# Kernel tuning notes

Measured on AMD Instinct MI355X. Metric: run time of the kernel, lower is better.

The kernel has to match this reference:

```python
import jax, jax.numpy as jnp
import numpy as np

B, L, E, H, D = 4, 2048, 2048, 16, 128
HALF = D // 2
EPS = 1e-6


def setup_inputs() -> dict:
    key = jax.random.key(0)
    ks = jax.random.split(key, 8)
    s = 1.0 / np.sqrt(E)
    x = jax.random.normal(ks[0], (B, L, E), dtype=jnp.float32)
    # causal boolean mask, True = attend
    attention_mask = jnp.tril(jnp.ones((L, L), dtype=bool))[None, None, :, :]
    attention_mask = jnp.broadcast_to(attention_mask, (B, 1, L, L))
    pos = jnp.arange(L, dtype=jnp.float32)[:, None]
    inv_freq = 1.0 / (10000.0 ** (jnp.arange(HALF, dtype=jnp.float32) / HALF))
    ang = pos * inv_freq[None, :]  # [L, HALF]
    cos = jnp.broadcast_to(jnp.cos(ang)[None], (B, L, HALF)).astype(jnp.float32)
    sin = jnp.broadcast_to(jnp.sin(ang)[None], (B, L, HALF)).astype(jnp.float32)
    Wq = jax.random.normal(ks[1], (H * D, E), dtype=jnp.float32) * s
    Wk = jax.random.normal(ks[2], (H * D, E), dtype=jnp.float32) * s
    Wv = jax.random.normal(ks[3], (H * D, E), dtype=jnp.float32) * s
    Wo = jax.random.normal(ks[4], (E, H * D), dtype=jnp.float32) * s
    q_norm_w = jnp.ones((D,), dtype=jnp.float32)
    k_norm_w = jnp.ones((D,), dtype=jnp.float32)
    return {"x": x, "attention_mask": attention_mask, "cos": cos, "sin": sin,
            "Wq": Wq, "Wk": Wk, "Wv": Wv, "Wo": Wo,
            "q_norm_w": q_norm_w, "k_norm_w": k_norm_w}


def _rmsnorm(t, w):
    # t: [B,H,L,D]; matches torch: x / sqrt(mean(x^2) + eps) * w
    ms = jnp.mean(t * t, axis=-1, keepdims=True)
    return w * (t * jax.lax.rsqrt(ms + EPS))


def _rope(t, cos, sin):
    # t: [B,H,L,D]; cos/sin: [B,L,HALF] -> [B,1,L,HALF]
    c = cos[:, None, :, :]
    s = sin[:, None, :, :]
    t1, t2 = t[..., :HALF], t[..., HALF:]
    return jnp.concatenate([t1 * c - t2 * s, t1 * s + t2 * c], axis=-1)


def reference(x, attention_mask, cos, sin, Wq, Wk, Wv, Wo, q_norm_w, k_norm_w):
    b, l, _ = x.shape
    q = (x @ Wq.T).reshape(b, l, H, D).transpose(0, 2, 1, 3)  # [B,H,L,D]
    k = (x @ Wk.T).reshape(b, l, H, D).transpose(0, 2, 1, 3)
    v = (x @ Wv.T).reshape(b, l, H, D).transpose(0, 2, 1, 3)
    q = _rope(_rmsnorm(q, q_norm_w), cos, sin)
    k = _rope(_rmsnorm(k, k_norm_w), cos, sin)
    scale = 1.0 / jnp.sqrt(jnp.asarray(D, dtype=x.dtype))
    scores = jnp.einsum('bhld,bhmd->bhlm', q, k) * scale  # [B,H,L,L]
    scores = jnp.where(attention_mask, scores, -jnp.inf)
    attn = jax.nn.softmax(scores, axis=-1)
    out = jnp.einsum('bhlm,bhmd->bhld', attn, v)  # [B,H,L,D]
    out = out.transpose(0, 2, 1, 3).reshape(b, l, H * D)
    return out @ Wo.T
```

## Files before the change

kernel.cpp:

```cpp
#include <hip/hip_runtime.h>
#include <hip/hip_bf16.h>
#include <stdint.h>

#define B_SZ 4
#define L_SEQ 2048
#define EMB 2048
#define NH 16
#define HD 128
#define BLROWS (B_SZ * L_SEQ)
#define BK 32

typedef __bf16 bf16;
typedef __bf16 bf16x8 __attribute__((ext_vector_type(8)));
typedef __bf16 bf16x4 __attribute__((ext_vector_type(4)));
typedef float f32x4 __attribute__((ext_vector_type(4)));

#define MFMA16(A, Bv, C) __builtin_amdgcn_mfma_f32_16x16x32_bf16(A, Bv, C, 0, 0, 0)

__device__ __forceinline__ void gll16(bf16* l, const bf16* g) {
  __builtin_amdgcn_global_load_lds(
      (const __attribute__((address_space(1))) unsigned int*)g,
      (__attribute__((address_space(3))) unsigned int*)l, 16, 0, 0);
}

__global__ __launch_bounds__(256) void f2b_kernel(const float* __restrict__ in,
                                                  bf16* __restrict__ out, int n4) {
  int i = blockIdx.x * blockDim.x + threadIdx.x;
  int stride = gridDim.x * blockDim.x;
  for (; i < n4; i += stride) {
    float4 v = ((const float4*)in)[i];
    bf16x4 o = {(bf16)v.x, (bf16)v.y, (bf16)v.z, (bf16)v.w};
    ((bf16x4*)out)[i] = o;
  }
}

template <int EPI>
__global__ __launch_bounds__(512, 2) void gemm256(const bf16* __restrict__ A,
                                                  const bf16* __restrict__ Bm,
                                                  bf16* __restrict__ Cq,
                                                  bf16* __restrict__ Ck,
                                                  bf16* __restrict__ Cvt,
                                                  float* __restrict__ Cf,
                                                  int K) {
  __shared__ bf16 Abuf[3][256 * BK];
  __shared__ bf16 Bbuf[3][256 * BK];
  const int tid = threadIdx.x, lane = tid & 63, w = tid >> 6;
  const int wr = w >> 2, wc = w & 3;
  const int l15 = lane & 15;

  const int q8 = gridDim.x >> 3;
  const int wg = ((int)blockIdx.x & 7) * q8 + ((int)blockIdx.x >> 3);
  const int bm = (wg & 31) * 256;
  const int bn = (wg >> 5) * 256;
  const int NT = K / BK;

  const int idA0 = tid, idA1 = 512 + tid;
  const int ar0 = idA0 >> 2, ar1 = idA1 >> 2;
  const size_t aS0 = (size_t)(bm + ar0) * K + (((idA0 & 3) ^ ((ar0 >> 1) & 3)) * 8);
  const size_t aS1 = (size_t)(bm + ar1) * K + (((idA1 & 3) ^ ((ar1 >> 1) & 3)) * 8);
  const size_t bS0 = (size_t)(bn + ar0) * K + (((idA0 & 3) ^ ((ar0 >> 1) & 3)) * 8);
  const size_t bS1 = (size_t)(bn + ar1) * K + (((idA1 & 3) ^ ((ar1 >> 1) & 3)) * 8);
  const int ldsD0 = idA0 * 8, ldsD1 = idA1 * 8;

  const int eSw = ((lane >> 4) * 8) ^ (((l15 >> 1) & 3) << 3);
  int aoff[8], boff[4];
#pragma unroll
  for (int m = 0; m < 8; m++) aoff[m] = (wr * 128 + m * 16 + l15) * BK + eSw;
#pragma unroll
  for (int n = 0; n < 4; n++) boff[n] = (wc * 64 + n * 16 + l15) * BK + eSw;

  f32x4 acc[8][4] = {};

  gll16(&Abuf[0][ldsD0], A + aS0);
  gll16(&Bbuf[0][ldsD0], Bm + bS0);
  gll16(&Abuf[0][ldsD1], A + aS1);
  gll16(&Bbuf[0][ldsD1], Bm + bS1);
  gll16(&Abuf[1][ldsD0], A + aS0 + BK);
  gll16(&Bbuf[1][ldsD0], Bm + bS0 + BK);
  gll16(&Abuf[1][ldsD1], A + aS1 + BK);
  gll16(&Bbuf[1][ldsD1], Bm + bS1 + BK);
  asm volatile("s_waitcnt vmcnt(4)" ::: "memory");
  __builtin_amdgcn_s_barrier();
  asm volatile("" ::: "memory");

  int cur = 0, nxt = 2;
  for (int kt = 0; kt < NT; ++kt) {
    const bf16* __restrict__ Ab = Abuf[cur];
    const bf16* __restrict__ Bb = Bbuf[cur];
    const bool pre = (kt + 2 < NT);
    const size_t k2 = (size_t)(kt + 2) * BK;

    bf16x8 af[8], b0, b1;
#pragma unroll
    for (int m = 0; m < 8; m++) af[m] = *(const bf16x8*)&Ab[aoff[m]];
    b0 = *(const bf16x8*)&Bb[boff[0]];
    b1 = *(const bf16x8*)&Bb[boff[1]];
    if (pre) {
      gll16(&Abuf[nxt][ldsD0], A + aS0 + k2);
      gll16(&Bbuf[nxt][ldsD0], Bm + bS0 + k2);
    }
    asm volatile("s_waitcnt lgkmcnt(0)" ::: "memory");
    __builtin_amdgcn_sched_barrier(0);
    __builtin_amdgcn_s_setprio(1);
#pragma unroll
    for (int m = 0; m < 8; m++) acc[m][0] = MFMA16(af[m], b0, acc[m][0]);
#pragma unroll
    for (int m = 0; m < 8; m++) acc[m][1] = MFMA16(af[m], b1, acc[m][1]);
    __builtin_amdgcn_s_setprio(0);

    bf16x8 b2 = *(const bf16x8*)&Bb[boff[2]];
    bf16x8 b3 = *(const bf16x8*)&Bb[boff[3]];
    if (pre) {
      gll16(&Abuf[nxt][ldsD1], A + aS1 + k2);
      gll16(&Bbuf[nxt][ldsD1], Bm + bS1 + k2);
    }
    asm volatile("s_waitcnt lgkmcnt(0)" ::: "memory");
    __builtin_amdgcn_sched_barrier(0);
    __builtin_amdgcn_s_setprio(1);
#pragma unroll
    for (int m = 0; m < 8; m++) acc[m][2] = MFMA16(af[m], b2, acc[m][2]);
#pragma unroll
    for (int m = 0; m < 8; m++) acc[m][3] = MFMA16(af[m], b3, acc[m][3]);
    __builtin_amdgcn_s_setprio(0);

    if (kt < NT - 1) {
      if (pre)
        asm volatile("s_waitcnt vmcnt(4)" ::: "memory");
      else
        asm volatile("s_waitcnt vmcnt(0)" ::: "memory");
      __builtin_amdgcn_s_barrier();
      asm volatile("" ::: "memory");
    }
    cur = (cur == 2) ? 0 : cur + 1;
    nxt = (nxt == 2) ? 0 : nxt + 1;
  }

  const int grow0 = bm + wr * 128 + (lane >> 4) * 4;
  const int gcol0 = bn + wc * 64 + l15;
#pragma unroll
  for (int i = 0; i < 8; i++)
#pragma unroll
    for (int j = 0; j < 4; j++) {
      int grow = grow0 + i * 16;
      int gcol = gcol0 + j * 16;
      if (EPI == 1) {
#pragma unroll
        for (int r = 0; r < 4; r++)
          Cf[(size_t)(grow + r) * 2048 + gcol] = acc[i][j][r];
      } else {
        int mat = gcol >> 11, mcol = gcol & 2047;
        if (mat == 2) {
          int b = grow >> 11;
          bf16x4 pk = {(bf16)acc[i][j][0], (bf16)acc[i][j][1],
                       (bf16)acc[i][j][2], (bf16)acc[i][j][3]};
          *(bf16x4*)&Cvt[((size_t)(b * 2048 + mcol)) * 2048 + (grow & 2047)] = pk;
        } else {
          bf16* Cp = (mat == 0) ? Cq : Ck;
#pragma unroll
          for (int r = 0; r < 4; r++)
            Cp[(size_t)(grow + r) * 2048 + mcol] = (bf16)acc[i][j][r];
        }
      }
    }
}

__global__ __launch_bounds__(256) void normrope_kernel(bf16* __restrict__ T,
                                                       const float* __restrict__ w,
                                                       const float* __restrict__ cs,
                                                       const float* __restrict__ sn) {
  int row = blockIdx.x * 4 + (threadIdx.x >> 6);
  int lane = threadIdx.x & 63;
  int bl = row >> 4;
  int h = row & 15;
  bf16* p = T + (size_t)bl * EMB + h * HD;
  float v1 = (float)p[lane];
  float v2 = (float)p[lane + 64];
  float ss = v1 * v1 + v2 * v2;
#pragma unroll
  for (int m = 32; m; m >>= 1) ss += __shfl_xor(ss, m, 64);
  float r = rsqrtf(ss * (1.0f / 128.0f) + 1e-6f);
  float n1 = v1 * r * w[lane];
  float n2 = v2 * r * w[lane + 64];
  float c = cs[(size_t)bl * 64 + lane];
  float s = sn[(size_t)bl * 64 + lane];
  p[lane]      = (bf16)(n1 * c - n2 * s);
  p[lane + 64] = (bf16)(n1 * s + n2 * c);
}

__device__ __forceinline__ void stage_kv(bf16* Ksb, bf16* Vsb,
                                         const bf16* gK, const bf16* gV,
                                         int kt, int w, int lane) {
#pragma unroll
  for (int i = 0; i < 4; i++) {
    int ck = i * 256 + w * 64 + lane;
    int kr = ck >> 4, kc = ck & 15;
    gll16(&Ksb[ck * 8], gK + (size_t)(kt * 64 + kr) * EMB + ((kc ^ (kr & 7)) * 8));
    int dr = ck >> 3, vc = ck & 7;
    gll16(&Vsb[ck * 8], gV + (size_t)dr * L_SEQ + kt * 64 + ((vc ^ (dr & 7)) * 8));
  }
}

__global__ __launch_bounds__(256) void fattn_kernel(const bf16* __restrict__ Q,
                                                    const bf16* __restrict__ K,
                                                    const bf16* __restrict__ Vt,
                                                    bf16* __restrict__ AO) {
  __shared__ bf16 Ks[2][64 * 128];
  __shared__ bf16 Vs[2][64 * 128];
  __shared__ bf16 Ps[4 * 32 * 64];
  const int tid = threadIdx.x, lane = tid & 63, w = tid >> 6;
  const int l15 = lane & 15;

  int id = blockIdx.x + blockIdx.y * 16;
  int bh = id & 63;
  int qti = 15 - (id >> 6);
  const int b = bh >> 4, h = bh & 15;
  const size_t base = (size_t)b * L_SEQ * EMB + h * HD;
  const bf16* gK = K + base;
  const bf16* gV = Vt + (size_t)(b * NH + h) * HD * L_SEQ;
  const int qrow0 = qti * 128 + w * 32;

  const float a_ = 0.08838834764831845f * 1.4426950408889634f;
  const float b_ = 12.0f * 1.4426950408889634f;

  bf16x8 qf[2][4];
#pragma unroll
  for (int mi = 0; mi < 2; mi++) {
    const bf16* qp = Q + base + (size_t)(qrow0 + mi * 16 + l15) * EMB + ((lane >> 4) * 8);
#pragma unroll
    for (int c = 0; c < 4; c++) qf[mi][c] = *(const bf16x8*)(qp + c * 32);
  }
  const bf16 one1 = (bf16)1.0f;
  const bf16x8 ones = {one1, one1, one1, one1, one1, one1, one1, one1};

  f32x4 O[2][8] = {};
  f32x4 lsum[2] = {};
  const int prow = (lane >> 4) * 4;
  bf16* myP = Ps + w * 2048;

  const int nkt = 2 * qti + 2;
  stage_kv(Ks[0], Vs[0], gK, gV, 0, w, lane);
  asm volatile("s_waitcnt vmcnt(0)" ::: "memory");
  __builtin_amdgcn_s_barrier();
  asm volatile("" ::: "memory");

  for (int kt = 0; kt < nkt; kt++) {
    const int cur = kt & 1;
    if (kt + 1 < nkt) stage_kv(Ks[cur ^ 1], Vs[cur ^ 1], gK, gV, kt + 1, w, lane);

    const bool active = (kt * 64 <= qrow0 + 31);
    if (active) {
      f32x4 S[2][4] = {};
      __builtin_amdgcn_s_setprio(1);
#pragma unroll
      for (int s = 0; s < 4; s++) {
        int row = s * 16 + l15;
#pragma unroll
        for (int c = 0; c < 4; c++) {
          int swc = (c * 4 + (lane >> 4)) ^ (row & 7);
          bf16x8 kf = *(const bf16x8*)&Ks[cur][row * 128 + swc * 8];
          S[0][s] = MFMA16(qf[0][c], kf, S[0][s]);
          S[1][s] = MFMA16(qf[1][c], kf, S[1][s]);
        }
      }
      __builtin_amdgcn_s_setprio(0);

#pragma unroll
      for (int mi = 0; mi < 2; mi++)
#pragma unroll
        for (int s = 0; s < 4; s++) {
          int kg = kt * 64 + s * 16 + l15;
#pragma unroll
          for (int r = 0; r < 4; r++) {
            int qg = qrow0 + mi * 16 + prow + r;
            float e = exp2f(S[mi][s][r] * a_ - b_);
            if (kg > qg) e = 0.f;
            int row = mi * 16 + prow + r;
            myP[(row * 64 + s * 16 + l15) ^ ((row & 7) << 3)] = (bf16)e;
          }
        }
      bf16x8 pf[2][2];
#pragma unroll
      for (int mi = 0; mi < 2; mi++)
#pragma unroll
        for (int kk = 0; kk < 2; kk++) {
          int row = mi * 16 + l15;
          int swc = (kk * 4 + (lane >> 4)) ^ (row & 7);
          pf[mi][kk] = *(const bf16x8*)&myP[row * 64 + swc * 8];
        }
      __builtin_amdgcn_s_setprio(1);
#pragma unroll
      for (int mi = 0; mi < 2; mi++) {
        lsum[mi] = MFMA16(pf[mi][0], ones, lsum[mi]);
        lsum[mi] = MFMA16(pf[mi][1], ones, lsum[mi]);
      }
#pragma unroll
      for (int ni = 0; ni < 8; ni++) {
#pragma unroll
        for (int kk = 0; kk < 2; kk++) {
          int drow = ni * 16 + l15;
          int swc = (kk * 4 + (lane >> 4)) ^ (drow & 7);
          bf16x8 vf = *(const bf16x8*)&Vs[cur][drow * 64 + swc * 8];
          O[0][ni] = MFMA16(pf[0][kk], vf, O[0][ni]);
          O[1][ni] = MFMA16(pf[1][kk], vf, O[1][ni]);
        }
      }
      __builtin_amdgcn_s_setprio(0);
    }

    asm volatile("s_waitcnt vmcnt(0)" ::: "memory");
    __builtin_amdgcn_s_barrier();
    asm volatile("" ::: "memory");
  }

#pragma unroll
  for (int mi = 0; mi < 2; mi++)
#pragma unroll
    for (int ni = 0; ni < 8; ni++) {
#pragma unroll
      for (int r = 0; r < 4; r++) {
        float o = O[mi][ni][r] / lsum[mi][r];
        int grow = qrow0 + mi * 16 + prow + r;
        AO[(size_t)(b * L_SEQ + grow) * EMB + h * HD + ni * 16 + l15] = (bf16)o;
      }
    }
}

extern "C" void kernel_launch(void* const* d_in, const int* in_sizes, int n_in,
                              void* d_out, int out_size, void* d_ws, size_t ws_size,
                              hipStream_t stream) {
  const float* x = (const float*)d_in[0];
  const float* cosp = (const float*)d_in[2];
  const float* sinp = (const float*)d_in[3];
  const float* Wq = (const float*)d_in[4];
  const float* Wk = (const float*)d_in[5];
  const float* Wv = (const float*)d_in[6];
  const float* Wo = (const float*)d_in[7];
  const float* qw = (const float*)d_in[8];
  const float* kw = (const float*)d_in[9];

  const size_t ACT = (size_t)BLROWS * EMB * sizeof(bf16);
  const size_t WGT = (size_t)EMB * EMB * sizeof(bf16);
  char* ws = (char*)d_ws;
  bf16* xb    = (bf16*)ws;          ws += ACT;
  bf16* WQKVb = (bf16*)ws;          ws += 3 * WGT;
  bf16* Wob   = (bf16*)ws;          ws += WGT;
  bf16* Qb    = (bf16*)ws;          ws += ACT;
  bf16* Kb    = (bf16*)ws;          ws += ACT;
  bf16* Vtb   = (bf16*)ws;          ws += ACT;
  bf16* AOb   = (bf16*)ws;          ws += ACT;

  f2b_kernel<<<2048, 256, 0, stream>>>(x, xb, BLROWS * EMB / 4);
  f2b_kernel<<<1024, 256, 0, stream>>>(Wq, WQKVb, EMB * EMB / 4);
  f2b_kernel<<<1024, 256, 0, stream>>>(Wk, WQKVb + (size_t)EMB * EMB, EMB * EMB / 4);
  f2b_kernel<<<1024, 256, 0, stream>>>(Wv, WQKVb + 2 * (size_t)EMB * EMB, EMB * EMB / 4);
  f2b_kernel<<<1024, 256, 0, stream>>>(Wo, Wob, EMB * EMB / 4);

  gemm256<0><<<768, 512, 0, stream>>>(xb, WQKVb, Qb, Kb, Vtb, nullptr, EMB);

  normrope_kernel<<<BLROWS * NH / 4, 256, 0, stream>>>(Qb, qw, cosp, sinp);
  normrope_kernel<<<BLROWS * NH / 4, 256, 0, stream>>>(Kb, kw, cosp, sinp);

  fattn_kernel<<<dim3(16, B_SZ * NH), 256, 0, stream>>>(Qb, Kb, Vtb, AOb);

  gemm256<1><<<256, 512, 0, stream>>>(AOb, Wob, nullptr, nullptr, nullptr,
                                      (float*)d_out, EMB);
}
```

Before: 529.8 us.

## Split KV tiles across waves in flash attention and merge partial results in LDS

Each attention block now covers 64 query rows instead of 128, so the grid doubles. The four waves form two query halves times two KV parities: each wave processes alternate KV tiles, and the two partial O/lsum accumulators are summed through LDS (reusing the K/V buffers) before normalizing and writing. This is meant to improve load balance and occupancy on the causal triangle and to cut the idle wave work on partially masked tiles. The cost is that each block reloads K/V for fewer query rows, roughly doubling KV traffic, plus an extra LDS reduction and barriers at the end.

```diff
diff --git a/kernel.cpp b/kernel.cpp
--- a/kernel.cpp
+++ b/kernel.cpp
@@ -209,15 +209,16 @@
   __shared__ bf16 Ps[4 * 32 * 64];
   const int tid = threadIdx.x, lane = tid & 63, w = tid >> 6;
   const int l15 = lane & 15;
-
-  int id = blockIdx.x + blockIdx.y * 16;
+  const int qh = w & 1, kp = w >> 1;
+
+  int id = blockIdx.x + blockIdx.y * 32;
   int bh = id & 63;
-  int qti = 15 - (id >> 6);
+  int qt = 31 - (id >> 6);
   const int b = bh >> 4, h = bh & 15;
   const size_t base = (size_t)b * L_SEQ * EMB + h * HD;
   const bf16* gK = K + base;
   const bf16* gV = Vt + (size_t)(b * NH + h) * HD * L_SEQ;
-  const int qrow0 = qti * 128 + w * 32;
+  const int qrow0 = qt * 64 + qh * 32;
 
   const float a_ = 0.08838834764831845f * 1.4426950408889634f;
   const float b_ = 12.0f * 1.4426950408889634f;
@@ -237,18 +238,16 @@
   const int prow = (lane >> 4) * 4;
   bf16* myP = Ps + w * 2048;
 
-  const int nkt = 2 * qti + 2;
   stage_kv(Ks[0], Vs[0], gK, gV, 0, w, lane);
   asm volatile("s_waitcnt vmcnt(0)" ::: "memory");
   __builtin_amdgcn_s_barrier();
   asm volatile("" ::: "memory");
 
-  for (int kt = 0; kt < nkt; kt++) {
+  for (int kt = 0; kt <= qt; kt++) {
     const int cur = kt & 1;
-    if (kt + 1 < nkt) stage_kv(Ks[cur ^ 1], Vs[cur ^ 1], gK, gV, kt + 1, w, lane);
-
-    const bool active = (kt * 64 <= qrow0 + 31);
-    if (active) {
+    if (kt < qt) stage_kv(Ks[cur ^ 1], Vs[cur ^ 1], gK, gV, kt + 1, w, lane);
+
+    if ((kt & 1) == kp) {
       f32x4 S[2][4] = {};
       __builtin_amdgcn_s_setprio(1);
 #pragma unroll
@@ -312,17 +311,41 @@
     asm volatile("" ::: "memory");
   }
 
-#pragma unroll
-  for (int mi = 0; mi < 2; mi++)
-#pragma unroll
-    for (int ni = 0; ni < 8; ni++) {
-#pragma unroll
-      for (int r = 0; r < 4; r++) {
-        float o = O[mi][ni][r] / lsum[mi][r];
-        int grow = qrow0 + mi * 16 + prow + r;
-        AO[(size_t)(b * L_SEQ + grow) * EMB + h * HD + ni * 16 + l15] = (bf16)o;
-      }
-    }
+  __syncthreads();
+  float* cO = (float*)Ks;
+  float* cL = (float*)Vs;
+  if (kp == 1) {
+#pragma unroll
+    for (int mi = 0; mi < 2; mi++) {
+#pragma unroll
+      for (int ni = 0; ni < 8; ni++)
+#pragma unroll
+        for (int r = 0; r < 4; r++)
+          cO[qh * 4096 + (mi * 16 + prow + r) * 128 + ni * 16 + l15] = O[mi][ni][r];
+      if (l15 == 0)
+#pragma unroll
+        for (int r = 0; r < 4; r++) cL[qh * 32 + mi * 16 + prow + r] = lsum[mi][r];
+    }
+  }
+  __syncthreads();
+  if (kp == 0) {
+#pragma unroll
+    for (int mi = 0; mi < 2; mi++) {
+      f32x4 lt;
+#pragma unroll
+      for (int r = 0; r < 4; r++)
+        lt[r] = lsum[mi][r] + cL[qh * 32 + mi * 16 + prow + r];
+#pragma unroll
+      for (int ni = 0; ni < 8; ni++)
+#pragma unroll
+        for (int r = 0; r < 4; r++) {
+          float o = (O[mi][ni][r] +
+                     cO[qh * 4096 + (mi * 16 + prow + r) * 128 + ni * 16 + l15]) / lt[r];
+          int grow = qrow0 + mi * 16 + prow + r;
+          AO[(size_t)(b * L_SEQ + grow) * EMB + h * HD + ni * 16 + l15] = (bf16)o;
+        }
+    }
+  }
 }
 
 extern "C" void kernel_launch(void* const* d_in, const int* in_sizes, int n_in,
@@ -360,7 +383,7 @@
   normrope_kernel<<<BLROWS * NH / 4, 256, 0, stream>>>(Qb, qw, cosp, sinp);
   normrope_kernel<<<BLROWS * NH / 4, 256, 0, stream>>>(Kb, kw, cosp, sinp);
 
-  fattn_kernel<<<dim3(16, B_SZ * NH), 256, 0, stream>>>(Qb, Kb, Vtb, AOb);
+  fattn_kernel<<<dim3(32, B_SZ * NH), 256, 0, stream>>>(Qb, Kb, Vtb, AOb);
 
   gemm256<1><<<256, 512, 0, stream>>>(AOb, Wob, nullptr, nullptr, nullptr,
                                       (float*)d_out, EMB);
```

Measured after the change: 695.2 us. 31.2% more time.
